# Optimization experiments

Hardware: AMD Instinct MI355X
Metric: run time of the kernel (lower is better)

Reference implementation:

```python
import jax, jax.numpy as jnp
import numpy as np

N_NODES = 100000
N_EDGES = 1600000
IN_DIM, HID_DIM, OUT_DIM = 128, 64, 1


def setup_inputs() -> dict:
    key = jax.random.key(0)
    ks = jax.random.split(key, 8)
    x = jax.random.normal(ks[0], (N_NODES, IN_DIM), dtype=jnp.float32)
    edge_index = jax.random.randint(ks[1], (2, N_EDGES), 0, N_NODES, dtype=jnp.int64)
    # Glorot-ish scaled weights
    W1 = jax.random.normal(ks[2], (IN_DIM, HID_DIM), dtype=jnp.float32) / np.sqrt(IN_DIM)
    b1 = jnp.zeros((HID_DIM,), dtype=jnp.float32)
    W2 = jax.random.normal(ks[3], (HID_DIM, HID_DIM), dtype=jnp.float32) / np.sqrt(HID_DIM)
    b2 = jnp.zeros((HID_DIM,), dtype=jnp.float32)
    W3 = jax.random.normal(ks[4], (HID_DIM, OUT_DIM), dtype=jnp.float32) / np.sqrt(HID_DIM)
    b3 = jnp.zeros((OUT_DIM,), dtype=jnp.float32)
    return {"x": x, "edge_index": edge_index, "W1": W1, "b1": b1,
            "W2": W2, "b2": b2, "W3": W3, "b3": b3}


def _gcn_norm(edge_index, num_nodes):
    # PyG gcn_norm with add_self_loops=True, edge_weight=1:
    # deg[i] = 1 (self loop) + #incoming edges at i (dst = edge_index[1])
    dst = edge_index[1]
    deg = jnp.ones((num_nodes,), dtype=jnp.float32).at[dst].add(1.0)
    dis = jnp.where(deg > 0, 1.0 / jnp.sqrt(deg), 0.0)  # deg_inv_sqrt
    return dis


def _gcn_conv(x, W, b, src, dst, dis):
    h = x @ W                                   # [N, F_out] transform first (PyG order)
    norm = dis[src] * dis[dst]                  # [E]
    msg = h[src] * norm[:, None]                # gather + scale, [E, F_out]
    out = jnp.zeros_like(h).at[dst].add(msg)    # scatter-add aggregation
    out = out + h * (dis * dis)[:, None]        # self-loop contribution
    return out + b


def reference(x, edge_index, W1, b1, W2, b2, W3, b3):
    src, dst = edge_index[0], edge_index[1]
    dis = _gcn_norm(edge_index, x.shape[0])
    h = jax.nn.relu(_gcn_conv(x, W1, b1, src, dst, dis))   # dropout = identity (eval)
    h = jax.nn.relu(_gcn_conv(h, W2, b2, src, dst, dis))
    return _gcn_conv(h, W3, b3, src, dst, dis)
```

## Files before the change

kernel.cpp:

```cpp
#include <hip/hip_runtime.h>

#define IN_DIM 128
#define HID 64
#define MAXC 400
#define EPB 8192
#define CAP 6144

static __device__ __forceinline__ unsigned short f2bf(float f) {
    unsigned u = __float_as_uint(f);
    u += 0x7FFF + ((u >> 16) & 1);
    return (unsigned short)(u >> 16);
}
static __device__ __forceinline__ float bf2f(unsigned short h) {
    return __uint_as_float((unsigned)h << 16);
}

typedef short bf16x8 __attribute__((ext_vector_type(8)));
typedef float f32x4 __attribute__((ext_vector_type(4)));

__global__ __launch_bounds__(256) void k_part1(const int* __restrict__ src,
                                               const int* __restrict__ dst,
                                               int* __restrict__ cursorC,
                                               int* __restrict__ tmp1,
                                               int E, int NC) {
    __shared__ int bcnt[MAXC];
    __shared__ int bbase[MAXC];
    int tid = threadIdx.x;
    int e0 = blockIdx.x * EPB;
    int e1 = min(e0 + EPB, E);
    for (int i = tid; i < NC; i += 256) bcnt[i] = 0;
    __syncthreads();
    for (int e = e0 + tid; e < e1; e += 256) atomicAdd(&bcnt[dst[e] >> 8], 1);
    __syncthreads();
    for (int i = tid; i < NC; i += 256) {
        int c = bcnt[i];
        bbase[i] = c ? atomicAdd(&cursorC[i], c) : 0;
    }
    __syncthreads();
    for (int i = tid; i < NC; i += 256) bcnt[i] = 0;
    __syncthreads();
    for (int e = e0 + tid; e < e1; e += 256) {
        int s = src[e], d = dst[e];
        int cb = d >> 8;
        int slot = bbase[cb] + atomicAdd(&bcnt[cb], 1);
        tmp1[(size_t)cb * CAP + slot] = s | ((d & 255) << 17);
    }
}

__global__ __launch_bounds__(512) void k_cscan(const int* __restrict__ cursorC,
                                               int* __restrict__ coarseStart,
                                               int* __restrict__ rowStart,
                                               int NC, int N, int E) {
    __shared__ int tmp[512];
    int t = threadIdx.x;
    int v = (t < NC) ? cursorC[t] : 0;
    tmp[t] = v;
    __syncthreads();
    for (int off = 1; off < 512; off <<= 1) {
        int a = (t >= off) ? tmp[t - off] : 0;
        __syncthreads();
        tmp[t] += a;
        __syncthreads();
    }
    int excl = tmp[t] - v;
    if (t < NC) coarseStart[t] = excl;
    if (t == NC - 1) coarseStart[NC] = excl + v;
    if (t == 0) rowStart[N] = E;
}

__global__ __launch_bounds__(256) void k_degplace(const int* __restrict__ tmp1,
                                                  const int* __restrict__ cursorC,
                                                  const int* __restrict__ coarseStart,
                                                  float* __restrict__ dis,
                                                  int* __restrict__ rowStart,
                                                  int* __restrict__ esrc, int N) {
    __shared__ int hist[256];
    __shared__ int scn[256];
    __shared__ int cur[256];
    int tid = threadIdx.x;
    int cb = blockIdx.x;
    int node0 = cb << 8;
    const int cnt = cursorC[cb];
    const size_t bp = (size_t)cb * CAP;
    const int g0 = coarseStart[cb];
    hist[tid] = 0;
    __syncthreads();
    for (int i = tid; i < cnt; i += 256)
        atomicAdd(&hist[((unsigned)tmp1[bp + i]) >> 17], 1);
    __syncthreads();
    int v = hist[tid];
    scn[tid] = v;
    __syncthreads();
    for (int off = 1; off < 256; off <<= 1) {
        int a = (tid >= off) ? scn[tid - off] : 0;
        __syncthreads();
        scn[tid] += a;
        __syncthreads();
    }
    int myStart = g0 + scn[tid] - v;
    cur[tid] = myStart;
    int node = node0 + tid;
    if (node < N) {
        dis[node] = rsqrtf((float)v + 1.0f);
        rowStart[node] = myStart;
    }
    __syncthreads();
    for (int i = tid; i < cnt; i += 256) {
        int pk = tmp1[bp + i];
        int dl = ((unsigned)pk) >> 17;
        int pos = atomicAdd(&cur[dl], 1);
        esrc[pos] = (pk & 0x1FFFF) << 7;
    }
}

template <int K>
__global__ __launch_bounds__(256) void k_mmx(const float* __restrict__ X,
                                             const float* __restrict__ W,
                                             const float* __restrict__ dis,
                                             unsigned short* __restrict__ Hbs, int N) {
    constexpr int WP = K + 8;
    __shared__ unsigned short Wt[64 * WP];
    const int tid = threadIdx.x;
    for (int i = tid; i < K * 64; i += 256) {
        int k = i >> 6, n = i & 63;
        Wt[n * WP + k] = f2bf(W[i]);
    }
    __syncthreads();
    const int lane = tid & 63;
    const int m16 = lane & 15;
    const int quad = lane >> 4;
    const int rowBase = blockIdx.x * 64 + (tid >> 6) * 16;
    const int rowc = min(rowBase + m16, N - 1);

    f32x4 acc0 = {0.f, 0.f, 0.f, 0.f};
    f32x4 acc1 = acc0, acc2 = acc0, acc3 = acc0;
    const float* xrow = X + (size_t)rowc * K;
#pragma unroll
    for (int k0 = 0; k0 < K; k0 += 32) {
        const float* xp = xrow + k0 + quad * 8;
        float4 xa = *(const float4*)xp;
        float4 xb = *(const float4*)(xp + 4);
        bf16x8 af;
        af[0] = (short)f2bf(xa.x); af[1] = (short)f2bf(xa.y);
        af[2] = (short)f2bf(xa.z); af[3] = (short)f2bf(xa.w);
        af[4] = (short)f2bf(xb.x); af[5] = (short)f2bf(xb.y);
        af[6] = (short)f2bf(xb.z); af[7] = (short)f2bf(xb.w);
        const unsigned short* wp = &Wt[m16 * WP + k0 + quad * 8];
        bf16x8 b0 = *(const bf16x8*)(wp);
        bf16x8 b1 = *(const bf16x8*)(wp + 16 * WP);
        bf16x8 b2 = *(const bf16x8*)(wp + 32 * WP);
        bf16x8 b3 = *(const bf16x8*)(wp + 48 * WP);
        acc0 = __builtin_amdgcn_mfma_f32_16x16x32_bf16(af, b0, acc0, 0, 0, 0);
        acc1 = __builtin_amdgcn_mfma_f32_16x16x32_bf16(af, b1, acc1, 0, 0, 0);
        acc2 = __builtin_amdgcn_mfma_f32_16x16x32_bf16(af, b2, acc2, 0, 0, 0);
        acc3 = __builtin_amdgcn_mfma_f32_16x16x32_bf16(af, b3, acc3, 0, 0, 0);
    }
#pragma unroll
    for (int reg = 0; reg < 4; ++reg) {
        int r = rowBase + quad * 4 + reg;
        if (r < N) {
            float dsc = dis[r];
            unsigned short* hp = Hbs + (size_t)r * 64 + m16;
            hp[0]  = f2bf(acc0[reg] * dsc);
            hp[16] = f2bf(acc1[reg] * dsc);
            hp[32] = f2bf(acc2[reg] * dsc);
            hp[48] = f2bf(acc3[reg] * dsc);
        }
    }
}

#define GNODE2(ACC, RA, RB)                                                    \
    {                                                                          \
        int j0 = max(RA - base, 0);                                            \
        int j1 = min(RB - base, cnt);                                          \
        int j = j0;                                                            \
        for (; j + 4 <= j1; j += 4) {                                          \
            unsigned o1 = __shfl(eoff, j + g, 64);                             \
            unsigned o2 = __shfl(eoff, j + 2 + g, 64);                         \
            unsigned d1 = *(const unsigned*)(hbase + o1);                      \
            unsigned d2 = *(const unsigned*)(hbase + o2);                      \
            ACC.x += __uint_as_float(d1 << 16);                                \
            ACC.y += __uint_as_float(d1 & 0xFFFF0000u);                        \
            ACC.x += __uint_as_float(d2 << 16);                                \
            ACC.y += __uint_as_float(d2 & 0xFFFF0000u);                        \
        }                                                                      \
        for (; j < j1; j += 2) {                                               \
            int idx = j + g;                                                   \
            bool valid = idx < j1;                                             \
            unsigned o = __shfl(eoff, valid ? idx : j0, 64);                   \
            unsigned d = *(const unsigned*)(hbase + o);                        \
            d = valid ? d : 0u;                                                \
            ACC.x += __uint_as_float(d << 16);                                 \
            ACC.y += __uint_as_float(d & 0xFFFF0000u);                         \
        }                                                                      \
    }

__global__ __launch_bounds__(256) void k_gather64(const unsigned short* __restrict__ Hbs,
                                                  const int* __restrict__ esrc,
                                                  const int* __restrict__ rowStart,
                                                  const float* __restrict__ dis,
                                                  const float* __restrict__ b,
                                                  float* __restrict__ out,
                                                  int N, int doRelu) {
    int lane = threadIdx.x & 63;
    int l = lane & 31;
    int g = lane >> 5;
    int wave = (blockIdx.x * 256 + threadIdx.x) >> 6;
    int g0 = wave * 4;
    if (g0 >= N) return;
    const char* hbase = (const char*)Hbs + l * 4;

    int rb = rowStart[min(g0 + lane, N)];
    int R0 = __shfl(rb, 0, 64), R1 = __shfl(rb, 1, 64);
    int R2 = __shfl(rb, 2, 64), R3 = __shfl(rb, 3, 64);
    int R4 = __shfl(rb, 4, 64);
    float dv = dis[min(g0 + lane, N - 1)];
    float d0 = __shfl(dv, 0, 64), d1 = __shfl(dv, 1, 64);
    float d2 = __shfl(dv, 2, 64), d3 = __shfl(dv, 3, 64);
    float2 bl = ((const float2*)b)[l];

    float2 a0 = {0.f, 0.f}, a1 = {0.f, 0.f}, a2 = {0.f, 0.f}, a3 = {0.f, 0.f};
    {
        int n0 = (g == 0) ? g0 : min(g0 + 2, N - 1);
        int n1 = (g == 0) ? min(g0 + 1, N - 1) : min(g0 + 3, N - 1);
        unsigned s0 = *(const unsigned*)(hbase + (size_t)n0 * 128);
        unsigned s1 = *(const unsigned*)(hbase + (size_t)n1 * 128);
        float2 f0 = {__uint_as_float(s0 << 16), __uint_as_float(s0 & 0xFFFF0000u)};
        float2 f1 = {__uint_as_float(s1 << 16), __uint_as_float(s1 & 0xFFFF0000u)};
        if (g == 0) { a0 = f0; a1 = f1; } else { a2 = f0; a3 = f1; }
    }

    for (int base = R0; base < R4; base += 64) {
        int cnt = min(64, R4 - base);
        unsigned eoff = (lane < cnt) ? (unsigned)esrc[base + lane] : 0u;
        GNODE2(a0, R0, R1)
        GNODE2(a1, R1, R2)
        GNODE2(a2, R2, R3)
        GNODE2(a3, R3, R4)
    }

    a0.x += __shfl_xor(a0.x, 32, 64); a0.y += __shfl_xor(a0.y, 32, 64);
    a1.x += __shfl_xor(a1.x, 32, 64); a1.y += __shfl_xor(a1.y, 32, 64);
    a2.x += __shfl_xor(a2.x, 32, 64); a2.y += __shfl_xor(a2.y, 32, 64);
    a3.x += __shfl_xor(a3.x, 32, 64); a3.y += __shfl_xor(a3.y, 32, 64);

    float2 v0 = {a0.x * d0 + bl.x, a0.y * d0 + bl.y};
    float2 v1 = {a1.x * d1 + bl.x, a1.y * d1 + bl.y};
    float2 v2 = {a2.x * d2 + bl.x, a2.y * d2 + bl.y};
    float2 v3 = {a3.x * d3 + bl.x, a3.y * d3 + bl.y};
    if (doRelu) {
        v0.x = fmaxf(v0.x, 0.f); v0.y = fmaxf(v0.y, 0.f);
        v1.x = fmaxf(v1.x, 0.f); v1.y = fmaxf(v1.y, 0.f);
        v2.x = fmaxf(v2.x, 0.f); v2.y = fmaxf(v2.y, 0.f);
        v3.x = fmaxf(v3.x, 0.f); v3.y = fmaxf(v3.y, 0.f);
    }
    if (g == 0) {
        ((float2*)(out + (size_t)g0 * 64))[l] = v0;
        if (g0 + 1 < N) ((float2*)(out + (size_t)(g0 + 1) * 64))[l] = v1;
    } else {
        if (g0 + 2 < N) ((float2*)(out + (size_t)(g0 + 2) * 64))[l] = v2;
        if (g0 + 3 < N) ((float2*)(out + (size_t)(g0 + 3) * 64))[l] = v3;
    }
}

__global__ __launch_bounds__(256) void k_mm1col(const float* __restrict__ H,
                                                const float* __restrict__ W3,
                                                const float* __restrict__ b3,
                                                const float* __restrict__ dis,
                                                float* __restrict__ colS,
                                                float* __restrict__ out, int N) {
    int lane = threadIdx.x & 63;
    int node = (blockIdx.x * 256 + threadIdx.x) >> 6;
    if (node >= N) return;
    float v = H[(size_t)node * 64 + lane] * W3[lane];
#pragma unroll
    for (int off = 32; off >= 1; off >>= 1) v += __shfl_down(v, off, 64);
    if (lane == 0) {
        float d = dis[node];
        colS[node] = v * d;
        out[node] = v * d * d + b3[0];
    }
}

__global__ __launch_bounds__(256) void k_gather1(const float* __restrict__ colS,
                                                 const int* __restrict__ esrc,
                                                 const int* __restrict__ rowStart,
                                                 const float* __restrict__ dis,
                                                 float* __restrict__ out, int N) {
    int i = blockIdx.x * 256 + threadIdx.x;
    if (i >= N) return;
    int r0 = rowStart[i], r1 = rowStart[i + 1];
    float acc = 0.0f;
    for (int e = r0; e < r1; ++e) acc += colS[((unsigned)esrc[e]) >> 7];
    out[i] += acc * dis[i];
}

extern "C" void kernel_launch(void* const* d_in, const int* in_sizes, int n_in,
                              void* d_out, int out_size, void* d_ws, size_t ws_size,
                              hipStream_t stream) {
    const float* x  = (const float*)d_in[0];
    const int*   ei = (const int*)d_in[1];
    const float* W1 = (const float*)d_in[2];
    const float* b1 = (const float*)d_in[3];
    const float* W2 = (const float*)d_in[4];
    const float* b2 = (const float*)d_in[5];
    const float* W3 = (const float*)d_in[6];
    const float* b3 = (const float*)d_in[7];
    float* out = (float*)d_out;

    const int N = in_sizes[0] / IN_DIM;
    const int E = in_sizes[1] / 2;
    const int* src = ei;
    const int* dst = ei + E;
    const int NC = (N + 255) >> 8;

    char* w = (char*)d_ws;
    auto alloc = [&](size_t bytes) {
        char* p = w;
        w += (bytes + 1023) & ~(size_t)1023;
        return p;
    };
    float*          dis        = (float*)alloc((size_t)N * 4);
    float*          bufB       = (float*)alloc((size_t)N * 64 * 4);
    float*          bufC       = (float*)alloc((size_t)N * 64 * 4);
    unsigned short* Hbs        = (unsigned short*)alloc((size_t)N * 64 * 2);
    float*          colS       = (float*)alloc((size_t)N * 4);
    int*            rowStart   = (int*)alloc((size_t)(N + 1) * 4);
    int*            cursorC    = (int*)alloc((size_t)MAXC * 4);
    int*            coarseStart= (int*)alloc((size_t)(MAXC + 1) * 4);
    int*            esrc       = (int*)alloc((size_t)E * 4);
    int*            tmp1       = (int*)alloc((size_t)MAXC * CAP * 4);

    const int NB_N  = (N + 255) / 256;
    const int NB_MX = (N + 63) / 64;
    const int NB_WV = (N * 64 + 255) / 256;
    const int NB_G4 = ((N + 3) / 4 * 64 + 255) / 256;
    const int NB_P  = (E + EPB - 1) / EPB;

    hipMemsetAsync(cursorC, 0, (size_t)MAXC * sizeof(int), stream);
    k_part1<<<NB_P, 256, 0, stream>>>(src, dst, cursorC, tmp1, E, NC);
    k_cscan<<<1, 512, 0, stream>>>(cursorC, coarseStart, rowStart, NC, N, E);
    k_degplace<<<NC, 256, 0, stream>>>(tmp1, cursorC, coarseStart, dis, rowStart, esrc, N);

    k_mmx<IN_DIM><<<NB_MX, 256, 0, stream>>>(x, W1, dis, Hbs, N);
    k_gather64<<<NB_G4, 256, 0, stream>>>(Hbs, esrc, rowStart, dis, b1, bufB, N, 1);

    k_mmx<HID><<<NB_MX, 256, 0, stream>>>(bufB, W2, dis, Hbs, N);
    k_gather64<<<NB_G4, 256, 0, stream>>>(Hbs, esrc, rowStart, dis, b2, bufC, N, 1);

    k_mm1col<<<NB_WV, 256, 0, stream>>>(bufC, W3, b3, dis, colS, out, N);
    k_gather1<<<NB_N, 256, 0, stream>>>(colS, esrc, rowStart, dis, out, N);
}
```

Baseline: 280.0 us.

## Fuse final projection into layer-2 gather, store bf16 intermediates, retune partitioning

The layer-1 gather now writes its relu output as bf16, and the layer-2 matmul reads bf16 directly, which halves intermediate traffic and removes a conversion. The layer-2 gather folds the 64-to-1 projection with W3 into its epilogue via a lane reduction, so the separate k_mm1col kernel and its fp32 buffer disappear. Edge partition blocks shrink from 8192 to 2048 edges for more parallelism, and the degree/placement kernel runs with 1024 threads per block. The bf16 intermediate adds rounding error.

```diff
diff --git a/kernel.cpp b/kernel.cpp
--- a/kernel.cpp
+++ b/kernel.cpp
@@ -3,16 +3,14 @@
 #define IN_DIM 128
 #define HID 64
 #define MAXC 400
-#define EPB 8192
+#define EPB 2048
 #define CAP 6144
+#define DPT 1024
 
 static __device__ __forceinline__ unsigned short f2bf(float f) {
     unsigned u = __float_as_uint(f);
     u += 0x7FFF + ((u >> 16) & 1);
     return (unsigned short)(u >> 16);
-}
-static __device__ __forceinline__ float bf2f(unsigned short h) {
-    return __uint_as_float((unsigned)h << 16);
 }
 
 typedef short bf16x8 __attribute__((ext_vector_type(8)));
@@ -68,7 +66,7 @@
     if (t == 0) rowStart[N] = E;
 }
 
-__global__ __launch_bounds__(256) void k_degplace(const int* __restrict__ tmp1,
+__global__ __launch_bounds__(DPT) void k_degplace(const int* __restrict__ tmp1,
                                                   const int* __restrict__ cursorC,
                                                   const int* __restrict__ coarseStart,
                                                   float* __restrict__ dis,
@@ -83,29 +81,32 @@
     const int cnt = cursorC[cb];
     const size_t bp = (size_t)cb * CAP;
     const int g0 = coarseStart[cb];
-    hist[tid] = 0;
-    __syncthreads();
-    for (int i = tid; i < cnt; i += 256)
+    if (tid < 256) hist[tid] = 0;
+    __syncthreads();
+    for (int i = tid; i < cnt; i += DPT)
         atomicAdd(&hist[((unsigned)tmp1[bp + i]) >> 17], 1);
     __syncthreads();
-    int v = hist[tid];
-    scn[tid] = v;
+    int v = 0;
+    if (tid < 256) { v = hist[tid]; scn[tid] = v; }
     __syncthreads();
     for (int off = 1; off < 256; off <<= 1) {
-        int a = (tid >= off) ? scn[tid - off] : 0;
+        int a = 0;
+        if (tid < 256 && tid >= off) a = scn[tid - off];
         __syncthreads();
-        scn[tid] += a;
+        if (tid < 256) scn[tid] += a;
         __syncthreads();
     }
-    int myStart = g0 + scn[tid] - v;
-    cur[tid] = myStart;
-    int node = node0 + tid;
-    if (node < N) {
-        dis[node] = rsqrtf((float)v + 1.0f);
-        rowStart[node] = myStart;
-    }
-    __syncthreads();
-    for (int i = tid; i < cnt; i += 256) {
+    if (tid < 256) {
+        int myStart = g0 + scn[tid] - v;
+        cur[tid] = myStart;
+        int node = node0 + tid;
+        if (node < N) {
+            dis[node] = rsqrtf((float)v + 1.0f);
+            rowStart[node] = myStart;
+        }
+    }
+    __syncthreads();
+    for (int i = tid; i < cnt; i += DPT) {
         int pk = tmp1[bp + i];
         int dl = ((unsigned)pk) >> 17;
         int pos = atomicAdd(&cur[dl], 1);
@@ -113,8 +114,8 @@
     }
 }
 
-template <int K>
-__global__ __launch_bounds__(256) void k_mmx(const float* __restrict__ X,
+template <int K, typename T>
+__global__ __launch_bounds__(256) void k_mmx(const T* __restrict__ X,
                                              const float* __restrict__ W,
                                              const float* __restrict__ dis,
                                              unsigned short* __restrict__ Hbs, int N) {
@@ -134,17 +135,21 @@
 
     f32x4 acc0 = {0.f, 0.f, 0.f, 0.f};
     f32x4 acc1 = acc0, acc2 = acc0, acc3 = acc0;
-    const float* xrow = X + (size_t)rowc * K;
+    const T* xrow = X + (size_t)rowc * K;
 #pragma unroll
     for (int k0 = 0; k0 < K; k0 += 32) {
-        const float* xp = xrow + k0 + quad * 8;
-        float4 xa = *(const float4*)xp;
-        float4 xb = *(const float4*)(xp + 4);
         bf16x8 af;
-        af[0] = (short)f2bf(xa.x); af[1] = (short)f2bf(xa.y);
-        af[2] = (short)f2bf(xa.z); af[3] = (short)f2bf(xa.w);
-        af[4] = (short)f2bf(xb.x); af[5] = (short)f2bf(xb.y);
-        af[6] = (short)f2bf(xb.z); af[7] = (short)f2bf(xb.w);
+        if constexpr (sizeof(T) == 4) {
+            const float* xp = (const float*)xrow + k0 + quad * 8;
+            float4 xa = *(const float4*)xp;
+            float4 xb = *(const float4*)(xp + 4);
+            af[0] = (short)f2bf(xa.x); af[1] = (short)f2bf(xa.y);
+            af[2] = (short)f2bf(xa.z); af[3] = (short)f2bf(xa.w);
+            af[4] = (short)f2bf(xb.x); af[5] = (short)f2bf(xb.y);
+            af[6] = (short)f2bf(xb.z); af[7] = (short)f2bf(xb.w);
+        } else {
+            af = *(const bf16x8*)((const unsigned short*)xrow + k0 + quad * 8);
+        }
         const unsigned short* wp = &Wt[m16 * WP + k0 + quad * 8];
         bf16x8 b0 = *(const bf16x8*)(wp);
         bf16x8 b1 = *(const bf16x8*)(wp + 16 * WP);
@@ -195,13 +200,18 @@
         }                                                                      \
     }
 
+template <int MODE>
 __global__ __launch_bounds__(256) void k_gather64(const unsigned short* __restrict__ Hbs,
                                                   const int* __restrict__ esrc,
                                                   const int* __restrict__ rowStart,
                                                   const float* __restrict__ dis,
                                                   const float* __restrict__ b,
-                                                  float* __restrict__ out,
-                                                  int N, int doRelu) {
+                                                  unsigned short* __restrict__ outB,
+                                                  const float* __restrict__ W3,
+                                                  const float* __restrict__ b3,
+                                                  float* __restrict__ colS,
+                                                  float* __restrict__ outF,
+                                                  int N) {
     int lane = threadIdx.x & 63;
     int l = lane & 31;
     int g = lane >> 5;
@@ -244,41 +254,45 @@
     a2.x += __shfl_xor(a2.x, 32, 64); a2.y += __shfl_xor(a2.y, 32, 64);
     a3.x += __shfl_xor(a3.x, 32, 64); a3.y += __shfl_xor(a3.y, 32, 64);
 
-    float2 v0 = {a0.x * d0 + bl.x, a0.y * d0 + bl.y};
-    float2 v1 = {a1.x * d1 + bl.x, a1.y * d1 + bl.y};
-    float2 v2 = {a2.x * d2 + bl.x, a2.y * d2 + bl.y};
-    float2 v3 = {a3.x * d3 + bl.x, a3.y * d3 + bl.y};
-    if (doRelu) {
-        v0.x = fmaxf(v0.x, 0.f); v0.y = fmaxf(v0.y, 0.f);
-        v1.x = fmaxf(v1.x, 0.f); v1.y = fmaxf(v1.y, 0.f);
-        v2.x = fmaxf(v2.x, 0.f); v2.y = fmaxf(v2.y, 0.f);
-        v3.x = fmaxf(v3.x, 0.f); v3.y = fmaxf(v3.y, 0.f);
-    }
-    if (g == 0) {
-        ((float2*)(out + (size_t)g0 * 64))[l] = v0;
-        if (g0 + 1 < N) ((float2*)(out + (size_t)(g0 + 1) * 64))[l] = v1;
+    float2 v0 = {fmaxf(a0.x * d0 + bl.x, 0.f), fmaxf(a0.y * d0 + bl.y, 0.f)};
+    float2 v1 = {fmaxf(a1.x * d1 + bl.x, 0.f), fmaxf(a1.y * d1 + bl.y, 0.f)};
+    float2 v2 = {fmaxf(a2.x * d2 + bl.x, 0.f), fmaxf(a2.y * d2 + bl.y, 0.f)};
+    float2 v3 = {fmaxf(a3.x * d3 + bl.x, 0.f), fmaxf(a3.y * d3 + bl.y, 0.f)};
+
+    if (MODE == 1) {
+        unsigned p0 = (unsigned)f2bf(v0.x) | ((unsigned)f2bf(v0.y) << 16);
+        unsigned p1 = (unsigned)f2bf(v1.x) | ((unsigned)f2bf(v1.y) << 16);
+        unsigned p2 = (unsigned)f2bf(v2.x) | ((unsigned)f2bf(v2.y) << 16);
+        unsigned p3 = (unsigned)f2bf(v3.x) | ((unsigned)f2bf(v3.y) << 16);
+        unsigned* ob = (unsigned*)outB;
+        if (g == 0) {
+            ob[(size_t)g0 * 32 + l] = p0;
+            if (g0 + 1 < N) ob[(size_t)(g0 + 1) * 32 + l] = p1;
+        } else {
+            if (g0 + 2 < N) ob[(size_t)(g0 + 2) * 32 + l] = p2;
+            if (g0 + 3 < N) ob[(size_t)(g0 + 3) * 32 + l] = p3;
+        }
     } else {
-        if (g0 + 2 < N) ((float2*)(out + (size_t)(g0 + 2) * 64))[l] = v2;
-        if (g0 + 3 < N) ((float2*)(out + (size_t)(g0 + 3) * 64))[l] = v3;
-    }
-}
-
-__global__ __launch_bounds__(256) void k_mm1col(const float* __restrict__ H,
-                                                const float* __restrict__ W3,
-                                                const float* __restrict__ b3,
-                                                const float* __restrict__ dis,
-                                                float* __restrict__ colS,
-                                                float* __restrict__ out, int N) {
-    int lane = threadIdx.x & 63;
-    int node = (blockIdx.x * 256 + threadIdx.x) >> 6;
-    if (node >= N) return;
-    float v = H[(size_t)node * 64 + lane] * W3[lane];
+        float2 w3 = ((const float2*)W3)[l];
+        float t0 = v0.x * w3.x + v0.y * w3.y;
+        float t1 = v1.x * w3.x + v1.y * w3.y;
+        float t2 = v2.x * w3.x + v2.y * w3.y;
+        float t3 = v3.x * w3.x + v3.y * w3.y;
 #pragma unroll
-    for (int off = 32; off >= 1; off >>= 1) v += __shfl_down(v, off, 64);
-    if (lane == 0) {
-        float d = dis[node];
-        colS[node] = v * d;
-        out[node] = v * d * d + b3[0];
+        for (int off = 1; off <= 16; off <<= 1) {
+            t0 += __shfl_xor(t0, off, 64);
+            t1 += __shfl_xor(t1, off, 64);
+            t2 += __shfl_xor(t2, off, 64);
+            t3 += __shfl_xor(t3, off, 64);
+        }
+        if (lane == 0) {
+            float bb = b3[0];
+            colS[g0] = t0 * d0;
+            outF[g0] = t0 * d0 * d0 + bb;
+            if (g0 + 1 < N) { colS[g0 + 1] = t1 * d1; outF[g0 + 1] = t1 * d1 * d1 + bb; }
+            if (g0 + 2 < N) { colS[g0 + 2] = t2 * d2; outF[g0 + 2] = t2 * d2 * d2 + bb; }
+            if (g0 + 3 < N) { colS[g0 + 3] = t3 * d3; outF[g0 + 3] = t3 * d3 * d3 + bb; }
+        }
     }
 }
 
@@ -321,9 +335,8 @@
         return p;
     };
     float*          dis        = (float*)alloc((size_t)N * 4);
-    float*          bufB       = (float*)alloc((size_t)N * 64 * 4);
-    float*          bufC       = (float*)alloc((size_t)N * 64 * 4);
     unsigned short* Hbs        = (unsigned short*)alloc((size_t)N * 64 * 2);
+    unsigned short* Hb1        = (unsigned short*)alloc((size_t)N * 64 * 2);
     float*          colS       = (float*)alloc((size_t)N * 4);
     int*            rowStart   = (int*)alloc((size_t)(N + 1) * 4);
     int*            cursorC    = (int*)alloc((size_t)MAXC * 4);
@@ -333,21 +346,21 @@
 
     const int NB_N  = (N + 255) / 256;
     const int NB_MX = (N + 63) / 64;
-    const int NB_WV = (N * 64 + 255) / 256;
     const int NB_G4 = ((N + 3) / 4 * 64 + 255) / 256;
     const int NB_P  = (E + EPB - 1) / EPB;
 
     hipMemsetAsync(cursorC, 0, (size_t)MAXC * sizeof(int), stream);
     k_part1<<<NB_P, 256, 0, stream>>>(src, dst, cursorC, tmp1, E, NC);
     k_cscan<<<1, 512, 0, stream>>>(cursorC, coarseStart, rowStart, NC, N, E);
-    k_degplace<<<NC, 256, 0, stream>>>(tmp1, cursorC, coarseStart, dis, rowStart, esrc, N);
-
-    k_mmx<IN_DIM><<<NB_MX, 256, 0, stream>>>(x, W1, dis, Hbs, N);
-    k_gather64<<<NB_G4, 256, 0, stream>>>(Hbs, esrc, rowStart, dis, b1, bufB, N, 1);
-
-    k_mmx<HID><<<NB_MX, 256, 0, stream>>>(bufB, W2, dis, Hbs, N);
-    k_gather64<<<NB_G4, 256, 0, stream>>>(Hbs, esrc, rowStart, dis, b2, bufC, N, 1);
-
-    k_mm1col<<<NB_WV, 256, 0, stream>>>(bufC, W3, b3, dis, colS, out, N);
+    k_degplace<<<NC, DPT, 0, stream>>>(tmp1, cursorC, coarseStart, dis, rowStart, esrc, N);
+
+    k_mmx<IN_DIM, float><<<NB_MX, 256, 0, stream>>>(x, W1, dis, Hbs, N);
+    k_gather64<1><<<NB_G4, 256, 0, stream>>>(Hbs, esrc, rowStart, dis, b1,
+                                             Hb1, nullptr, nullptr, nullptr, nullptr, N);
+
+    k_mmx<HID, unsigned short><<<NB_MX, 256, 0, stream>>>(Hb1, W2, dis, Hbs, N);
+    k_gather64<2><<<NB_G4, 256, 0, stream>>>(Hbs, esrc, rowStart, dis, b2,
+                                             nullptr, W3, b3, colS, out, N);
+
     k_gather1<<<NB_N, 256, 0, stream>>>(colS, esrc, rowStart, dis, out, N);
 }
```

New measurement: 270.0 us. 3.6% less time.
